# Optimization experiments

Hardware: AMD Instinct MI355X
Metric: run time of the kernel (lower is better)

Reference implementation:

```python
import jax, jax.numpy as jnp
import numpy as np

B = 16384
N_NARR = 128
N_SUB = 1024
K = N_SUB // N_NARR  # narrative i -> subnarratives [i*K, (i+1)*K)
GAMMA = 2.0
NW, SW, HW = 1.0, 1.0, 0.5  # narrative/subnarrative/hierarchy weights


def setup_inputs() -> dict:
    key = jax.random.key(0)
    k1, k2, k3, k4 = jax.random.split(key, 4)
    return {
        "narrative_logits": jax.random.normal(k1, (B, N_NARR), jnp.float32),
        "subnarrative_logits": jax.random.normal(k2, (B, N_SUB), jnp.float32),
        "narrative_labels": jax.random.randint(k3, (B, N_NARR), 0, 2, jnp.int32),
        "subnarrative_labels": jax.random.randint(k4, (B, N_SUB), 0, 2, jnp.int32),
    }


def _weighted_bce(logits, labels, pos_weight):
    # BCEWithLogits with pos_weight: pw*y*softplus(-x) + (1-y)*softplus(x)
    return pos_weight * labels * jax.nn.softplus(-logits) + (1.0 - labels) * jax.nn.softplus(logits)


def reference(narrative_logits, subnarrative_logits, narrative_labels, subnarrative_labels):
    nl = narrative_labels.astype(jnp.float32)
    sl = subnarrative_labels.astype(jnp.float32)
    b = narrative_logits.shape[0]

    # class-balanced pos_weights, clamped to [1, 50]
    npw = jnp.clip((1.0 - nl).sum(0) / (nl.sum(0) + 1e-6), 1.0, 50.0)
    spw = jnp.clip((1.0 - sl).sum(0) / (sl.sum(0) + 1e-6), 1.0, 50.0)

    narrative_loss = _weighted_bce(narrative_logits, nl, npw).mean()

    # ragged subnarrative loss, vectorized: groups of K subnarrs per narrative.
    # per-(sample, positive-narrative) mean BCE over the group, averaged over
    # the number of valid (sample, narrative) pairs -- same math as the loop.
    sub_bce = _weighted_bce(subnarrative_logits, sl, spw).reshape(b, N_NARR, K)
    per_group = sub_bce.mean(-1)              # [B, N_NARR]
    pos = nl                                   # positive-narrative mask [B, N_NARR]
    valid_count = pos.sum()
    subnarrative_loss = jnp.where(
        valid_count > 0, (per_group * pos).sum() / jnp.maximum(valid_count, 1.0), 0.0)

    # hierarchy consistency: relu(max subnarr prob - narr prob) over positives
    nprob = jax.nn.sigmoid(narrative_logits)
    sprob = jax.nn.sigmoid(subnarrative_logits)
    grp_max = sprob.reshape(b, N_NARR, K).max(-1)  # [B, N_NARR]
    hierarchy_loss = (jax.nn.relu(grp_max - nprob) * pos).sum() / b

    # focal terms (mean over all elements)
    nf = ((1.0 - nprob) ** GAMMA * nl * jax.nn.log_sigmoid(narrative_logits)).mean()
    sf = ((1.0 - sprob) ** GAMMA * sl * jax.nn.log_sigmoid(subnarrative_logits)).mean()

    total = (NW * (narrative_loss - 0.1 * nf)
             + SW * (subnarrative_loss - 0.1 * sf)
             + HW * hierarchy_loss)
    return total
```

## Files before the change

kernel.cpp:

```cpp
#include <hip/hip_runtime.h>


#define BDIM 256
#define NROWS 16384
#define NNARR 128
#define NSUB 1024
#define ROWS_PER_BLOCK 16
#define NBLOCKS (NROWS / ROWS_PER_BLOCK)

#define WS_AN    0
#define WS_CN    128
#define WS_NSUM  256
#define WS_AS    384
#define WS_CS    1408
#define WS_SSUM  2432
#define WS_FN    3456
#define WS_FS    3457
#define WS_HIER  3458
#define WS_FLOATS 3459
#define CSTRIDE  3472
#define NCHUNK_MAX 32

__device__ __forceinline__ void bce_pieces(float x, float& sp_p, float& sp_m, float& sig) {
    float a = fabsf(x);
    float e = __expf(-a);
    float l = __logf(1.0f + e);
    sp_p = fmaxf(x, 0.0f) + l;
    sp_m = sp_p - x;
    float inv = __builtin_amdgcn_rcpf(1.0f + e);
    sig = (x >= 0.0f) ? inv : e * inv;
}

__device__ __forceinline__ void emit4(float* dst, float a, float b, float c, float d, int excl) {
    if (excl) {
        *(float4*)dst = make_float4(a, b, c, d);
    } else {
        atomicAdd(dst + 0, a); atomicAdd(dst + 1, b);
        atomicAdd(dst + 2, c); atomicAdd(dst + 3, d);
    }
}

__global__ __launch_bounds__(BDIM, 4) void ncl_main(
    const float* __restrict__ nlog, const float* __restrict__ slog,
    const int*   __restrict__ nlab, const int*   __restrict__ slab,
    float* __restrict__ ws, int ncopies, int excl)
{
    __shared__ float sred[BDIM][13];
    __shared__ float ssc[4][3];

    const int t  = threadIdx.x;
    const int r0 = blockIdx.x * ROWS_PER_BLOCK;
    float* const cw = ws + (size_t)(blockIdx.x % ncopies) * CSTRIDE;

    float fn = 0.f, fs = 0.f, hier = 0.f;

    {
        float An[4] = {0,0,0,0}, Cn[4] = {0,0,0,0}, ns[4] = {0,0,0,0};
        #pragma unroll
        for (int i = 0; i < 2; ++i) {
            const int base = r0 * NNARR + 4 * (i * BDIM + t);
            const float4 xs = *(const float4*)(nlog + base);
            const int4   ys = *(const int4*)  (nlab + base);
            const float xv[4] = {xs.x, xs.y, xs.z, xs.w};
            const float yv[4] = {(float)ys.x, (float)ys.y, (float)ys.z, (float)ys.w};
            #pragma unroll
            for (int j = 0; j < 4; ++j) {
                float sp_p, sp_m, sig;
                bce_pieces(xv[j], sp_p, sp_m, sig);
                float y = yv[j];
                An[j] += y * sp_m;
                Cn[j] += (1.0f - y) * sp_p;
                ns[j] += y;
                float om = 1.0f - sig;
                fn += om * om * y * (-sp_m);
            }
        }
        #pragma unroll
        for (int j = 0; j < 4; ++j) {
            sred[t][j] = An[j]; sred[t][4 + j] = Cn[j]; sred[t][8 + j] = ns[j];
        }
    }
    __syncthreads();
    if (t < 32) {
        float a[12];
        #pragma unroll
        for (int j = 0; j < 12; ++j) a[j] = sred[t][j];
        #pragma unroll
        for (int s = 1; s < 8; ++s)
            #pragma unroll
            for (int j = 0; j < 12; ++j) a[j] += sred[t + 32 * s][j];
        emit4(cw + WS_AN   + 4 * t, a[0], a[1], a[2],  a[3],  excl);
        emit4(cw + WS_CN   + 4 * t, a[4], a[5], a[6],  a[7],  excl);
        emit4(cw + WS_NSUM + 4 * t, a[8], a[9], a[10], a[11], excl);
    }

    const int g = t >> 1;
    float As[4] = {0,0,0,0}, Cs[4] = {0,0,0,0}, ss[4] = {0,0,0,0};
    #pragma unroll 4
    for (int i = 0; i < ROWS_PER_BLOCK; ++i) {
        const int r = r0 + i;
        const float  nx   = nlog[r * NNARR + g];
        const float  posv = (float)nlab[r * NNARR + g];
        const float4 xs = *(const float4*)(slog + r * NSUB + 4 * t);
        const int4   ys = *(const int4*)  (slab + r * NSUB + 4 * t);

        float nsig;
        {
            float a = fabsf(nx);
            float e = __expf(-a);
            float inv = __builtin_amdgcn_rcpf(1.0f + e);
            nsig = (nx >= 0.0f) ? inv : e * inv;
        }

        const float xv[4] = {xs.x, xs.y, xs.z, xs.w};
        const float yv[4] = {(float)ys.x, (float)ys.y, (float)ys.z, (float)ys.w};
        float mymax = 0.0f;
        #pragma unroll
        for (int j = 0; j < 4; ++j) {
            float sp_p, sp_m, sig;
            bce_pieces(xv[j], sp_p, sp_m, sig);
            float y = yv[j];
            As[j] += posv * y * sp_m;
            Cs[j] += posv * (1.0f - y) * sp_p;
            ss[j] += y;
            float om = 1.0f - sig;
            fs += om * om * y * (-sp_m);
            mymax = fmaxf(mymax, sig);
        }
        float gmax = fmaxf(mymax, __shfl_xor(mymax, 1, 64));
        if ((t & 1) == 0)
            hier += fmaxf(gmax - nsig, 0.0f) * posv;
    }

    emit4(cw + WS_AS   + 4 * t, As[0], As[1], As[2], As[3], excl);
    emit4(cw + WS_CS   + 4 * t, Cs[0], Cs[1], Cs[2], Cs[3], excl);
    emit4(cw + WS_SSUM + 4 * t, ss[0], ss[1], ss[2], ss[3], excl);

    #pragma unroll
    for (int off = 32; off; off >>= 1) {
        fn   += __shfl_down(fn,   off, 64);
        fs   += __shfl_down(fs,   off, 64);
        hier += __shfl_down(hier, off, 64);
    }
    if ((t & 63) == 0) {
        int w = t >> 6;
        ssc[w][0] = fn; ssc[w][1] = fs; ssc[w][2] = hier;
    }
    __syncthreads();
    if (t == 0) {
        float a = 0.f, b = 0.f, c = 0.f;
        #pragma unroll
        for (int w = 0; w < 4; ++w) { a += ssc[w][0]; b += ssc[w][1]; c += ssc[w][2]; }
        if (excl) {
            cw[WS_FN] = a; cw[WS_FS] = b; cw[WS_HIER] = c;
        } else {
            atomicAdd(cw + WS_FN, a); atomicAdd(cw + WS_FS, b); atomicAdd(cw + WS_HIER, c);
        }
    }
}

__global__ __launch_bounds__(256) void ncl_reduce1(const float* __restrict__ ws,
                                                   float* __restrict__ tmp,
                                                   int ncopies)
{
    const int e = blockIdx.x * 256 + threadIdx.x;
    if (e >= WS_FLOATS) return;
    const int c0 = blockIdx.y * NCHUNK_MAX;
    const int c1 = min(c0 + NCHUNK_MAX, ncopies);
    float s = 0.f;
    for (int c = c0; c < c1; ++c)
        s += ws[(size_t)c * CSTRIDE + e];
    tmp[(size_t)blockIdx.y * CSTRIDE + e] = s;
}

__global__ __launch_bounds__(256) void ncl_reduce2(const float* __restrict__ tmp,
                                                   float* __restrict__ red,
                                                   int nchunks)
{
    const int e = blockIdx.x * 256 + threadIdx.x;
    if (e >= WS_FLOATS) return;
    float s = 0.f;
    for (int c = 0; c < nchunks; ++c)
        s += tmp[(size_t)c * CSTRIDE + e];
    red[e] = s;
}

__global__ __launch_bounds__(1024) void ncl_finalize(const float* __restrict__ ws,
                                                     float* __restrict__ out)
{
    __shared__ float sr[3][16];
    const int t = threadIdx.x;
    const float Bf = (float)NROWS;

    float s_sub = ws[WS_SSUM + t];
    float spw   = fminf(fmaxf((Bf - s_sub) / (s_sub + 1e-6f), 1.0f), 50.0f);
    float sub_part = spw * ws[WS_AS + t] + ws[WS_CS + t];

    float narr_part = 0.f, valid_part = 0.f;
    if (t < NNARR) {
        float s = ws[WS_NSUM + t];
        float npw = fminf(fmaxf((Bf - s) / (s + 1e-6f), 1.0f), 50.0f);
        narr_part  = npw * ws[WS_AN + t] + ws[WS_CN + t];
        valid_part = s;
    }

    #pragma unroll
    for (int off = 32; off; off >>= 1) {
        sub_part   += __shfl_down(sub_part,   off, 64);
        narr_part  += __shfl_down(narr_part,  off, 64);
        valid_part += __shfl_down(valid_part, off, 64);
    }
    if ((t & 63) == 0) {
        int w = t >> 6;
        sr[0][w] = sub_part; sr[1][w] = narr_part; sr[2][w] = valid_part;
    }
    __syncthreads();
    if (t == 0) {
        float sub_tot = 0.f, narr_tot = 0.f, valid = 0.f;
        #pragma unroll
        for (int i = 0; i < 16; ++i) { sub_tot += sr[0][i]; narr_tot += sr[1][i]; valid += sr[2][i]; }

        float narrative_loss = narr_tot / (Bf * (float)NNARR);
        float sub_loss = (valid > 0.0f) ? (sub_tot * (1.0f / 8.0f)) / fmaxf(valid, 1.0f) : 0.0f;
        float nf = ws[WS_FN] / (Bf * (float)NNARR);
        float sf = ws[WS_FS] / (Bf * (float)NSUB);
        float hier_loss = ws[WS_HIER] / Bf;

        out[0] = (narrative_loss - 0.1f * nf)
               + (sub_loss       - 0.1f * sf)
               + 0.5f * hier_loss;
    }
}

extern "C" void kernel_launch(void* const* d_in, const int* in_sizes, int n_in,
                              void* d_out, int out_size, void* d_ws, size_t ws_size,
                              hipStream_t stream) {
    const float* nlog = (const float*)d_in[0];
    const float* slog = (const float*)d_in[1];
    const int*   nlab = (const int*)d_in[2];
    const int*   slab = (const int*)d_in[3];
    float* ws  = (float*)d_ws;
    float* out = (float*)d_out;

    long avail = (long)(ws_size / 4);
    long nc = avail / CSTRIDE - (NCHUNK_MAX + 1);
    int ncopies = (int)(nc < 1 ? 1 : (nc > NBLOCKS ? NBLOCKS : nc));
    int excl = (ncopies == NBLOCKS) ? 1 : 0;
    float* tmp = ws + (size_t)ncopies * CSTRIDE;
    float* red = tmp + (size_t)NCHUNK_MAX * CSTRIDE;
    int nchunks = (ncopies + NCHUNK_MAX - 1) / NCHUNK_MAX;

    if (!excl)
        hipMemsetAsync(ws, 0, (size_t)ncopies * CSTRIDE * sizeof(float), stream);

    ncl_main<<<NBLOCKS, BDIM, 0, stream>>>(nlog, slog, nlab, slab, ws, ncopies, excl);

    dim3 g1((WS_FLOATS + 255) / 256, nchunks);
    ncl_reduce1<<<g1, 256, 0, stream>>>(ws, tmp, ncopies);
    ncl_reduce2<<<(WS_FLOATS + 255) / 256, 256, 0, stream>>>(tmp, red, nchunks);
    ncl_finalize<<<1, 1024, 0, stream>>>(red, out);
}
```

Baseline: 191.5 us.

## Tile work by column slices to reduce per-block partials to a single atomic workspace

Each block now covers a 32-column slice of subnarratives (4 narratives) across 256 rows, instead of 16 full rows. Column partials are reduced inside the block with wave shuffles and LDS, then atomically added into one small workspace. This replaces the multi-copy workspace and the two reduction kernels with a single memset. The price is strided row access (128-byte segments per row) and more contended atomics, 2048 blocks per column slot.

```diff
diff --git a/kernel.cpp b/kernel.cpp
--- a/kernel.cpp
+++ b/kernel.cpp
@@ -5,8 +5,14 @@
 #define NROWS 16384
 #define NNARR 128
 #define NSUB 1024
-#define ROWS_PER_BLOCK 16
-#define NBLOCKS (NROWS / ROWS_PER_BLOCK)
+
+#define NSLICES 32
+#define SUBC 32
+#define NARRC 4
+#define ROWS_PER_CHUNK 256
+#define NCHUNKS (NROWS / ROWS_PER_CHUNK)
+#define NBLOCKS (NCHUNKS * NSLICES)
+#define ITERS (ROWS_PER_CHUNK / 32)
 
 #define WS_AN    0
 #define WS_CN    128
@@ -18,8 +24,6 @@
 #define WS_FS    3457
 #define WS_HIER  3458
 #define WS_FLOATS 3459
-#define CSTRIDE  3472
-#define NCHUNK_MAX 32
 
 __device__ __forceinline__ void bce_pieces(float x, float& sp_p, float& sp_m, float& sig) {
     float a = fabsf(x);
@@ -31,158 +35,134 @@
     sig = (x >= 0.0f) ? inv : e * inv;
 }
 
-__device__ __forceinline__ void emit4(float* dst, float a, float b, float c, float d, int excl) {
-    if (excl) {
-        *(float4*)dst = make_float4(a, b, c, d);
-    } else {
-        atomicAdd(dst + 0, a); atomicAdd(dst + 1, b);
-        atomicAdd(dst + 2, c); atomicAdd(dst + 3, d);
-    }
-}
-
-__global__ __launch_bounds__(BDIM, 4) void ncl_main(
+__global__ __launch_bounds__(BDIM, 6) void ncl_main(
     const float* __restrict__ nlog, const float* __restrict__ slog,
     const int*   __restrict__ nlab, const int*   __restrict__ slab,
-    float* __restrict__ ws, int ncopies, int excl)
+    float* __restrict__ ws)
 {
-    __shared__ float sred[BDIM][13];
-    __shared__ float ssc[4][3];
-
-    const int t  = threadIdx.x;
-    const int r0 = blockIdx.x * ROWS_PER_BLOCK;
-    float* const cw = ws + (size_t)(blockIdx.x % ncopies) * CSTRIDE;
-
-    float fn = 0.f, fs = 0.f, hier = 0.f;
-
-    {
-        float An[4] = {0,0,0,0}, Cn[4] = {0,0,0,0}, ns[4] = {0,0,0,0};
-        #pragma unroll
-        for (int i = 0; i < 2; ++i) {
-            const int base = r0 * NNARR + 4 * (i * BDIM + t);
-            const float4 xs = *(const float4*)(nlog + base);
-            const int4   ys = *(const int4*)  (nlab + base);
-            const float xv[4] = {xs.x, xs.y, xs.z, xs.w};
-            const float yv[4] = {(float)ys.x, (float)ys.y, (float)ys.z, (float)ys.w};
-            #pragma unroll
-            for (int j = 0; j < 4; ++j) {
-                float sp_p, sp_m, sig;
-                bce_pieces(xv[j], sp_p, sp_m, sig);
-                float y = yv[j];
-                An[j] += y * sp_m;
-                Cn[j] += (1.0f - y) * sp_p;
-                ns[j] += y;
-                float om = 1.0f - sig;
-                fn += om * om * y * (-sp_m);
-            }
-        }
-        #pragma unroll
-        for (int j = 0; j < 4; ++j) {
-            sred[t][j] = An[j]; sred[t][4 + j] = Cn[j]; sred[t][8 + j] = ns[j];
-        }
-    }
-    __syncthreads();
-    if (t < 32) {
-        float a[12];
-        #pragma unroll
-        for (int j = 0; j < 12; ++j) a[j] = sred[t][j];
-        #pragma unroll
-        for (int s = 1; s < 8; ++s)
-            #pragma unroll
-            for (int j = 0; j < 12; ++j) a[j] += sred[t + 32 * s][j];
-        emit4(cw + WS_AN   + 4 * t, a[0], a[1], a[2],  a[3],  excl);
-        emit4(cw + WS_CN   + 4 * t, a[4], a[5], a[6],  a[7],  excl);
-        emit4(cw + WS_NSUM + 4 * t, a[8], a[9], a[10], a[11], excl);
-    }
-
-    const int g = t >> 1;
-    float As[4] = {0,0,0,0}, Cs[4] = {0,0,0,0}, ss[4] = {0,0,0,0};
-    #pragma unroll 4
-    for (int i = 0; i < ROWS_PER_BLOCK; ++i) {
-        const int r = r0 + i;
-        const float  nx   = nlog[r * NNARR + g];
-        const float  posv = (float)nlab[r * NNARR + g];
-        const float4 xs = *(const float4*)(slog + r * NSUB + 4 * t);
-        const int4   ys = *(const int4*)  (slab + r * NSUB + 4 * t);
-
-        float nsig;
-        {
-            float a = fabsf(nx);
-            float e = __expf(-a);
-            float inv = __builtin_amdgcn_rcpf(1.0f + e);
-            nsig = (nx >= 0.0f) ? inv : e * inv;
-        }
+    __shared__ float lsub[4][8][12];
+    __shared__ float lnar[4][4][3];
+    __shared__ float lsc[4][3];
+
+    const int t     = threadIdx.x;
+    const int j     = blockIdx.x & (NSLICES - 1);
+    const int chunk = blockIdx.x >> 5;
+    const int q  = t & 7;
+    const int ro = t >> 3;
+    const int cl = q >> 1;
+    const bool evenq = (q & 1) == 0;
+
+    const int r0 = chunk * ROWS_PER_CHUNK + ro;
+    const float* sp = slog + (size_t)r0 * NSUB  + j * SUBC  + 4 * q;
+    const int*   yp = slab + (size_t)r0 * NSUB  + j * SUBC  + 4 * q;
+    const float* np = nlog + (size_t)r0 * NNARR + j * NARRC + cl;
+    const int*   mp = nlab + (size_t)r0 * NNARR + j * NARRC + cl;
+
+    float As[4] = {0,0,0,0}, Cs[4] = {0,0,0,0}, ssum[4] = {0,0,0,0};
+    float An = 0.f, Cn = 0.f, ns = 0.f, fn = 0.f, fs = 0.f, hier = 0.f;
+
+    #pragma unroll 2
+    for (int it = 0; it < ITERS; ++it) {
+        const size_t so = (size_t)it * 32 * NSUB;
+        const size_t no = (size_t)it * 32 * NNARR;
+        const float4 xs = *(const float4*)(sp + so);
+        const int4   ys = *(const int4*)  (yp + so);
+        const float  nx   = np[no];
+        const float  posv = (float)mp[no];
+
+        float nsp_p, nsp_m, nsig;
+        bce_pieces(nx, nsp_p, nsp_m, nsig);
 
         const float xv[4] = {xs.x, xs.y, xs.z, xs.w};
         const float yv[4] = {(float)ys.x, (float)ys.y, (float)ys.z, (float)ys.w};
         float mymax = 0.0f;
         #pragma unroll
-        for (int j = 0; j < 4; ++j) {
+        for (int k = 0; k < 4; ++k) {
             float sp_p, sp_m, sig;
-            bce_pieces(xv[j], sp_p, sp_m, sig);
-            float y = yv[j];
-            As[j] += posv * y * sp_m;
-            Cs[j] += posv * (1.0f - y) * sp_p;
-            ss[j] += y;
+            bce_pieces(xv[k], sp_p, sp_m, sig);
+            float y = yv[k];
+            As[k]   += posv * y * sp_m;
+            Cs[k]   += posv * (1.0f - y) * sp_p;
+            ssum[k] += y;
             float om = 1.0f - sig;
             fs += om * om * y * (-sp_m);
             mymax = fmaxf(mymax, sig);
         }
         float gmax = fmaxf(mymax, __shfl_xor(mymax, 1, 64));
-        if ((t & 1) == 0)
+        if (evenq) {
             hier += fmaxf(gmax - nsig, 0.0f) * posv;
-    }
-
-    emit4(cw + WS_AS   + 4 * t, As[0], As[1], As[2], As[3], excl);
-    emit4(cw + WS_CS   + 4 * t, Cs[0], Cs[1], Cs[2], Cs[3], excl);
-    emit4(cw + WS_SSUM + 4 * t, ss[0], ss[1], ss[2], ss[3], excl);
+            An += posv * nsp_m;
+            Cn += (1.0f - posv) * nsp_p;
+            ns += posv;
+            float om = 1.0f - nsig;
+            fn += om * om * posv * (-nsp_m);
+        }
+    }
 
     #pragma unroll
-    for (int off = 32; off; off >>= 1) {
-        fn   += __shfl_down(fn,   off, 64);
-        fs   += __shfl_down(fs,   off, 64);
-        hier += __shfl_down(hier, off, 64);
-    }
-    if ((t & 63) == 0) {
-        int w = t >> 6;
-        ssc[w][0] = fn; ssc[w][1] = fs; ssc[w][2] = hier;
-    }
+    for (int m = 8; m <= 32; m <<= 1) {
+        #pragma unroll
+        for (int k = 0; k < 4; ++k) {
+            As[k]   += __shfl_xor(As[k],   m, 64);
+            Cs[k]   += __shfl_xor(Cs[k],   m, 64);
+            ssum[k] += __shfl_xor(ssum[k], m, 64);
+        }
+        An += __shfl_xor(An, m, 64);
+        Cn += __shfl_xor(Cn, m, 64);
+        ns += __shfl_xor(ns, m, 64);
+    }
+    #pragma unroll
+    for (int m = 1; m <= 32; m <<= 1) {
+        fn   += __shfl_xor(fn,   m, 64);
+        fs   += __shfl_xor(fs,   m, 64);
+        hier += __shfl_xor(hier, m, 64);
+    }
+
+    const int w = t >> 6, lane = t & 63;
+    if (lane < 8) {
+        #pragma unroll
+        for (int k = 0; k < 4; ++k) {
+            lsub[w][lane][k]     = As[k];
+            lsub[w][lane][4 + k] = Cs[k];
+            lsub[w][lane][8 + k] = ssum[k];
+        }
+        if ((lane & 1) == 0) {
+            lnar[w][lane >> 1][0] = An;
+            lnar[w][lane >> 1][1] = Cn;
+            lnar[w][lane >> 1][2] = ns;
+        }
+    }
+    if (lane == 0) { lsc[w][0] = fn; lsc[w][1] = fs; lsc[w][2] = hier; }
     __syncthreads();
-    if (t == 0) {
-        float a = 0.f, b = 0.f, c = 0.f;
-        #pragma unroll
-        for (int w = 0; w < 4; ++w) { a += ssc[w][0]; b += ssc[w][1]; c += ssc[w][2]; }
-        if (excl) {
-            cw[WS_FN] = a; cw[WS_FS] = b; cw[WS_HIER] = c;
-        } else {
-            atomicAdd(cw + WS_FN, a); atomicAdd(cw + WS_FS, b); atomicAdd(cw + WS_HIER, c);
-        }
-    }
-}
-
-__global__ __launch_bounds__(256) void ncl_reduce1(const float* __restrict__ ws,
-                                                   float* __restrict__ tmp,
-                                                   int ncopies)
-{
-    const int e = blockIdx.x * 256 + threadIdx.x;
-    if (e >= WS_FLOATS) return;
-    const int c0 = blockIdx.y * NCHUNK_MAX;
-    const int c1 = min(c0 + NCHUNK_MAX, ncopies);
-    float s = 0.f;
-    for (int c = c0; c < c1; ++c)
-        s += ws[(size_t)c * CSTRIDE + e];
-    tmp[(size_t)blockIdx.y * CSTRIDE + e] = s;
-}
-
-__global__ __launch_bounds__(256) void ncl_reduce2(const float* __restrict__ tmp,
-                                                   float* __restrict__ red,
-                                                   int nchunks)
-{
-    const int e = blockIdx.x * 256 + threadIdx.x;
-    if (e >= WS_FLOATS) return;
-    float s = 0.f;
-    for (int c = 0; c < nchunks; ++c)
-        s += tmp[(size_t)c * CSTRIDE + e];
-    red[e] = s;
+
+    if (t < 8) {
+        float a[12];
+        #pragma unroll
+        for (int k = 0; k < 12; ++k)
+            a[k] = lsub[0][t][k] + lsub[1][t][k] + lsub[2][t][k] + lsub[3][t][k];
+        const int col = j * SUBC + 4 * t;
+        #pragma unroll
+        for (int k = 0; k < 4; ++k) {
+            atomicAdd(ws + WS_AS   + col + k, a[k]);
+            atomicAdd(ws + WS_CS   + col + k, a[4 + k]);
+            atomicAdd(ws + WS_SSUM + col + k, a[8 + k]);
+        }
+    } else if (t < 12) {
+        const int c = t - 8;
+        float a0 = lnar[0][c][0] + lnar[1][c][0] + lnar[2][c][0] + lnar[3][c][0];
+        float a1 = lnar[0][c][1] + lnar[1][c][1] + lnar[2][c][1] + lnar[3][c][1];
+        float a2 = lnar[0][c][2] + lnar[1][c][2] + lnar[2][c][2] + lnar[3][c][2];
+        atomicAdd(ws + WS_AN   + j * NARRC + c, a0);
+        atomicAdd(ws + WS_CN   + j * NARRC + c, a1);
+        atomicAdd(ws + WS_NSUM + j * NARRC + c, a2);
+    } else if (t == 12) {
+        float a = lsc[0][0] + lsc[1][0] + lsc[2][0] + lsc[3][0];
+        float b = lsc[0][1] + lsc[1][1] + lsc[2][1] + lsc[3][1];
+        float c = lsc[0][2] + lsc[1][2] + lsc[2][2] + lsc[3][2];
+        atomicAdd(ws + WS_FN,   a);
+        atomicAdd(ws + WS_FS,   b);
+        atomicAdd(ws + WS_HIER, c);
+    }
 }
 
 __global__ __launch_bounds__(1024) void ncl_finalize(const float* __restrict__ ws,
@@ -242,21 +222,7 @@
     float* ws  = (float*)d_ws;
     float* out = (float*)d_out;
 
-    long avail = (long)(ws_size / 4);
-    long nc = avail / CSTRIDE - (NCHUNK_MAX + 1);
-    int ncopies = (int)(nc < 1 ? 1 : (nc > NBLOCKS ? NBLOCKS : nc));
-    int excl = (ncopies == NBLOCKS) ? 1 : 0;
-    float* tmp = ws + (size_t)ncopies * CSTRIDE;
-    float* red = tmp + (size_t)NCHUNK_MAX * CSTRIDE;
-    int nchunks = (ncopies + NCHUNK_MAX - 1) / NCHUNK_MAX;
-
-    if (!excl)
-        hipMemsetAsync(ws, 0, (size_t)ncopies * CSTRIDE * sizeof(float), stream);
-
-    ncl_main<<<NBLOCKS, BDIM, 0, stream>>>(nlog, slog, nlab, slab, ws, ncopies, excl);
-
-    dim3 g1((WS_FLOATS + 255) / 256, nchunks);
-    ncl_reduce1<<<g1, 256, 0, stream>>>(ws, tmp, ncopies);
-    ncl_reduce2<<<(WS_FLOATS + 255) / 256, 256, 0, stream>>>(tmp, red, nchunks);
-    ncl_finalize<<<1, 1024, 0, stream>>>(red, out);
-}
+    hipMemsetAsync(ws, 0, WS_FLOATS * sizeof(float), stream);
+    ncl_main<<<NBLOCKS, BDIM, 0, stream>>>(nlog, slog, nlab, slab, ws);
+    ncl_finalize<<<1, 1024, 0, stream>>>(ws, out);
+}
```

Result: slower. 234.4 us (+22.4%).

## Drop atomics path, use per-block partials and merge reduce2 into finalize

Applied to the files above, without the earlier changes.

The main kernel now always writes per-block partials with plain vector stores, and the atomic fallback, its memset and the ncopies logic are removed. When the workspace is large enough it launches 2048 blocks of 8 rows instead of 1024 blocks of 16, and the occupancy hint rises to 6. The second reduction kernel is folded into finalize, which sums the 32 chunk partials itself, cutting one launch. The risk is that the small-workspace path assumes room for 1024 full partial copies without checking.

```diff
diff --git a/kernel.cpp b/kernel.cpp
--- a/kernel.cpp
+++ b/kernel.cpp
@@ -5,8 +5,6 @@
 #define NROWS 16384
 #define NNARR 128
 #define NSUB 1024
-#define ROWS_PER_BLOCK 16
-#define NBLOCKS (NROWS / ROWS_PER_BLOCK)
 
 #define WS_AN    0
 #define WS_CN    128
@@ -19,7 +17,8 @@
 #define WS_HIER  3458
 #define WS_FLOATS 3459
 #define CSTRIDE  3472
-#define NCHUNK_MAX 32
+
+#define NCHUNK 32
 
 __device__ __forceinline__ void bce_pieces(float x, float& sp_p, float& sp_m, float& sig) {
     float a = fabsf(x);
@@ -31,33 +30,25 @@
     sig = (x >= 0.0f) ? inv : e * inv;
 }
 
-__device__ __forceinline__ void emit4(float* dst, float a, float b, float c, float d, int excl) {
-    if (excl) {
-        *(float4*)dst = make_float4(a, b, c, d);
-    } else {
-        atomicAdd(dst + 0, a); atomicAdd(dst + 1, b);
-        atomicAdd(dst + 2, c); atomicAdd(dst + 3, d);
-    }
-}
-
-__global__ __launch_bounds__(BDIM, 4) void ncl_main(
+template<int RPB>
+__global__ __launch_bounds__(BDIM, 6) void ncl_main(
     const float* __restrict__ nlog, const float* __restrict__ slog,
     const int*   __restrict__ nlab, const int*   __restrict__ slab,
-    float* __restrict__ ws, int ncopies, int excl)
+    float* __restrict__ P)
 {
     __shared__ float sred[BDIM][13];
     __shared__ float ssc[4][3];
 
     const int t  = threadIdx.x;
-    const int r0 = blockIdx.x * ROWS_PER_BLOCK;
-    float* const cw = ws + (size_t)(blockIdx.x % ncopies) * CSTRIDE;
+    const int r0 = blockIdx.x * RPB;
+    float* const Pb = P + (size_t)blockIdx.x * CSTRIDE;
 
     float fn = 0.f, fs = 0.f, hier = 0.f;
 
     {
         float An[4] = {0,0,0,0}, Cn[4] = {0,0,0,0}, ns[4] = {0,0,0,0};
         #pragma unroll
-        for (int i = 0; i < 2; ++i) {
+        for (int i = 0; i < RPB / 8; ++i) {
             const int base = r0 * NNARR + 4 * (i * BDIM + t);
             const float4 xs = *(const float4*)(nlog + base);
             const int4   ys = *(const int4*)  (nlab + base);
@@ -89,20 +80,20 @@
         for (int s = 1; s < 8; ++s)
             #pragma unroll
             for (int j = 0; j < 12; ++j) a[j] += sred[t + 32 * s][j];
-        emit4(cw + WS_AN   + 4 * t, a[0], a[1], a[2],  a[3],  excl);
-        emit4(cw + WS_CN   + 4 * t, a[4], a[5], a[6],  a[7],  excl);
-        emit4(cw + WS_NSUM + 4 * t, a[8], a[9], a[10], a[11], excl);
+        *(float4*)(Pb + WS_AN   + 4 * t) = make_float4(a[0], a[1], a[2],  a[3]);
+        *(float4*)(Pb + WS_CN   + 4 * t) = make_float4(a[4], a[5], a[6],  a[7]);
+        *(float4*)(Pb + WS_NSUM + 4 * t) = make_float4(a[8], a[9], a[10], a[11]);
     }
 
     const int g = t >> 1;
     float As[4] = {0,0,0,0}, Cs[4] = {0,0,0,0}, ss[4] = {0,0,0,0};
     #pragma unroll 4
-    for (int i = 0; i < ROWS_PER_BLOCK; ++i) {
+    for (int i = 0; i < RPB; ++i) {
         const int r = r0 + i;
         const float  nx   = nlog[r * NNARR + g];
         const float  posv = (float)nlab[r * NNARR + g];
-        const float4 xs = *(const float4*)(slog + r * NSUB + 4 * t);
-        const int4   ys = *(const int4*)  (slab + r * NSUB + 4 * t);
+        const float4 xs = *(const float4*)(slog + (size_t)r * NSUB + 4 * t);
+        const int4   ys = *(const int4*)  (slab + (size_t)r * NSUB + 4 * t);
 
         float nsig;
         {
@@ -132,9 +123,9 @@
             hier += fmaxf(gmax - nsig, 0.0f) * posv;
     }
 
-    emit4(cw + WS_AS   + 4 * t, As[0], As[1], As[2], As[3], excl);
-    emit4(cw + WS_CS   + 4 * t, Cs[0], Cs[1], Cs[2], Cs[3], excl);
-    emit4(cw + WS_SSUM + 4 * t, ss[0], ss[1], ss[2], ss[3], excl);
+    *(float4*)(Pb + WS_AS   + 4 * t) = make_float4(As[0], As[1], As[2], As[3]);
+    *(float4*)(Pb + WS_CS   + 4 * t) = make_float4(Cs[0], Cs[1], Cs[2], Cs[3]);
+    *(float4*)(Pb + WS_SSUM + 4 * t) = make_float4(ss[0], ss[1], ss[2], ss[3]);
 
     #pragma unroll
     for (int off = 32; off; off >>= 1) {
@@ -151,57 +142,60 @@
         float a = 0.f, b = 0.f, c = 0.f;
         #pragma unroll
         for (int w = 0; w < 4; ++w) { a += ssc[w][0]; b += ssc[w][1]; c += ssc[w][2]; }
-        if (excl) {
-            cw[WS_FN] = a; cw[WS_FS] = b; cw[WS_HIER] = c;
-        } else {
-            atomicAdd(cw + WS_FN, a); atomicAdd(cw + WS_FS, b); atomicAdd(cw + WS_HIER, c);
-        }
-    }
-}
-
-__global__ __launch_bounds__(256) void ncl_reduce1(const float* __restrict__ ws,
+        Pb[WS_FN] = a; Pb[WS_FS] = b; Pb[WS_HIER] = c;
+    }
+}
+
+__global__ __launch_bounds__(256) void ncl_reduce1(const float* __restrict__ P,
                                                    float* __restrict__ tmp,
-                                                   int ncopies)
+                                                   int tpg)
 {
     const int e = blockIdx.x * 256 + threadIdx.x;
     if (e >= WS_FLOATS) return;
-    const int c0 = blockIdx.y * NCHUNK_MAX;
-    const int c1 = min(c0 + NCHUNK_MAX, ncopies);
+    const int g = blockIdx.y;
+    const float* p = P + (size_t)g * tpg * CSTRIDE + e;
     float s = 0.f;
-    for (int c = c0; c < c1; ++c)
-        s += ws[(size_t)c * CSTRIDE + e];
-    tmp[(size_t)blockIdx.y * CSTRIDE + e] = s;
-}
-
-__global__ __launch_bounds__(256) void ncl_reduce2(const float* __restrict__ tmp,
-                                                   float* __restrict__ red,
-                                                   int nchunks)
-{
-    const int e = blockIdx.x * 256 + threadIdx.x;
-    if (e >= WS_FLOATS) return;
-    float s = 0.f;
-    for (int c = 0; c < nchunks; ++c)
-        s += tmp[(size_t)c * CSTRIDE + e];
-    red[e] = s;
-}
-
-__global__ __launch_bounds__(1024) void ncl_finalize(const float* __restrict__ ws,
+    #pragma unroll 4
+    for (int i = 0; i < tpg; ++i)
+        s += p[(size_t)i * CSTRIDE];
+    tmp[(size_t)g * CSTRIDE + e] = s;
+}
+
+__global__ __launch_bounds__(1024) void ncl_finalize(const float* __restrict__ tmp,
                                                      float* __restrict__ out)
 {
-    __shared__ float sr[3][16];
+    __shared__ float sr[6][16];
     const int t = threadIdx.x;
     const float Bf = (float)NROWS;
 
-    float s_sub = ws[WS_SSUM + t];
-    float spw   = fminf(fmaxf((Bf - s_sub) / (s_sub + 1e-6f), 1.0f), 50.0f);
-    float sub_part = spw * ws[WS_AS + t] + ws[WS_CS + t];
+    float As = 0.f, Csv = 0.f, ss = 0.f;
+    #pragma unroll 4
+    for (int gc = 0; gc < NCHUNK; ++gc) {
+        const float* p = tmp + (size_t)gc * CSTRIDE;
+        As  += p[WS_AS   + t];
+        Csv += p[WS_CS   + t];
+        ss  += p[WS_SSUM + t];
+    }
+    float spw = fminf(fmaxf((Bf - ss) / (ss + 1e-6f), 1.0f), 50.0f);
+    float sub_part = spw * As + Csv;
 
     float narr_part = 0.f, valid_part = 0.f;
     if (t < NNARR) {
-        float s = ws[WS_NSUM + t];
-        float npw = fminf(fmaxf((Bf - s) / (s + 1e-6f), 1.0f), 50.0f);
-        narr_part  = npw * ws[WS_AN + t] + ws[WS_CN + t];
-        valid_part = s;
+        float An = 0.f, Cn = 0.f, ns = 0.f;
+        #pragma unroll 4
+        for (int gc = 0; gc < NCHUNK; ++gc) {
+            const float* p = tmp + (size_t)gc * CSTRIDE;
+            An += p[WS_AN + t]; Cn += p[WS_CN + t]; ns += p[WS_NSUM + t];
+        }
+        float npw = fminf(fmaxf((Bf - ns) / (ns + 1e-6f), 1.0f), 50.0f);
+        narr_part  = npw * An + Cn;
+        valid_part = ns;
+    }
+
+    float fn_p = 0.f, fs_p = 0.f, hier_p = 0.f;
+    if (t < NCHUNK) {
+        const float* p = tmp + (size_t)t * CSTRIDE;
+        fn_p = p[WS_FN]; fs_p = p[WS_FS]; hier_p = p[WS_HIER];
     }
 
     #pragma unroll
@@ -209,22 +203,30 @@
         sub_part   += __shfl_down(sub_part,   off, 64);
         narr_part  += __shfl_down(narr_part,  off, 64);
         valid_part += __shfl_down(valid_part, off, 64);
+        fn_p       += __shfl_down(fn_p,       off, 64);
+        fs_p       += __shfl_down(fs_p,       off, 64);
+        hier_p     += __shfl_down(hier_p,     off, 64);
     }
     if ((t & 63) == 0) {
         int w = t >> 6;
         sr[0][w] = sub_part; sr[1][w] = narr_part; sr[2][w] = valid_part;
+        sr[3][w] = fn_p;     sr[4][w] = fs_p;      sr[5][w] = hier_p;
     }
     __syncthreads();
     if (t == 0) {
         float sub_tot = 0.f, narr_tot = 0.f, valid = 0.f;
-        #pragma unroll
-        for (int i = 0; i < 16; ++i) { sub_tot += sr[0][i]; narr_tot += sr[1][i]; valid += sr[2][i]; }
+        float fn = 0.f, fs = 0.f, hier = 0.f;
+        #pragma unroll
+        for (int i = 0; i < 16; ++i) {
+            sub_tot += sr[0][i]; narr_tot += sr[1][i]; valid += sr[2][i];
+            fn += sr[3][i]; fs += sr[4][i]; hier += sr[5][i];
+        }
 
         float narrative_loss = narr_tot / (Bf * (float)NNARR);
         float sub_loss = (valid > 0.0f) ? (sub_tot * (1.0f / 8.0f)) / fmaxf(valid, 1.0f) : 0.0f;
-        float nf = ws[WS_FN] / (Bf * (float)NNARR);
-        float sf = ws[WS_FS] / (Bf * (float)NSUB);
-        float hier_loss = ws[WS_HIER] / Bf;
+        float nf = fn / (Bf * (float)NNARR);
+        float sf = fs / (Bf * (float)NSUB);
+        float hier_loss = hier / Bf;
 
         out[0] = (narrative_loss - 0.1f * nf)
                + (sub_loss       - 0.1f * sf)
@@ -239,24 +241,21 @@
     const float* slog = (const float*)d_in[1];
     const int*   nlab = (const int*)d_in[2];
     const int*   slab = (const int*)d_in[3];
-    float* ws  = (float*)d_ws;
+    float* P   = (float*)d_ws;
     float* out = (float*)d_out;
 
-    long avail = (long)(ws_size / 4);
-    long nc = avail / CSTRIDE - (NCHUNK_MAX + 1);
-    int ncopies = (int)(nc < 1 ? 1 : (nc > NBLOCKS ? NBLOCKS : nc));
-    int excl = (ncopies == NBLOCKS) ? 1 : 0;
-    float* tmp = ws + (size_t)ncopies * CSTRIDE;
-    float* red = tmp + (size_t)NCHUNK_MAX * CSTRIDE;
-    int nchunks = (ncopies + NCHUNK_MAX - 1) / NCHUNK_MAX;
-
-    if (!excl)
-        hipMemsetAsync(ws, 0, (size_t)ncopies * CSTRIDE * sizeof(float), stream);
-
-    ncl_main<<<NBLOCKS, BDIM, 0, stream>>>(nlog, slog, nlab, slab, ws, ncopies, excl);
-
-    dim3 g1((WS_FLOATS + 255) / 256, nchunks);
-    ncl_reduce1<<<g1, 256, 0, stream>>>(ws, tmp, ncopies);
-    ncl_reduce2<<<(WS_FLOATS + 255) / 256, 256, 0, stream>>>(tmp, red, nchunks);
-    ncl_finalize<<<1, 1024, 0, stream>>>(red, out);
-}
+    const size_t availf = ws_size / 4;
+    const bool big = availf >= (size_t)(2048 + NCHUNK) * CSTRIDE;
+    const int nblocks = big ? 2048 : 1024;
+    float* tmp = P + (size_t)nblocks * CSTRIDE;
+    const int tpg = nblocks / NCHUNK;
+
+    if (big)
+        ncl_main<8><<<2048, BDIM, 0, stream>>>(nlog, slog, nlab, slab, P);
+    else
+        ncl_main<16><<<1024, BDIM, 0, stream>>>(nlog, slog, nlab, slab, P);
+
+    dim3 gr((WS_FLOATS + 255) / 256, NCHUNK);
+    ncl_reduce1<<<gr, 256, 0, stream>>>(P, tmp, tpg);
+    ncl_finalize<<<1, 1024, 0, stream>>>(tmp, out);
+}
```

New measurement: 186.3 us. 1.03x faster.
